# Performance work log

Hardware: AMD Instinct MI355X
Metric: run time of the kernel (lower is better)

The kernel has to match this reference:

```python
import jax, jax.numpy as jnp
import numpy as np

K_MASK = jnp.finfo(jnp.bfloat16).min
ROPE_THETA = 1000000.0


def _rope_sincos(position_ids, head_dim, theta):
    # position_ids: [b, t] int -> sin, cos: [b, t, head_dim//2]
    frac = jnp.arange(0, head_dim, 2, dtype=jnp.float32) / head_dim
    timescale = theta ** frac
    ang = position_ids[..., None].astype(jnp.float32) / timescale
    return jnp.sin(ang), jnp.cos(ang)


def _apply_rope(x, sin, cos):
    # x: [b, t, n, h]; sin/cos: [b, t, h//2]
    h = x.shape[-1]
    x1, x2 = x[..., : h // 2], x[..., h // 2 :]
    s = sin[:, :, None, :]
    c = cos[:, :, None, :]
    return jnp.concatenate([x1 * c - x2 * s, x2 * c + x1 * s], axis=-1).astype(x.dtype)


def setup_inputs() -> dict:
    key = jax.random.key(0)
    ks = jax.random.split(key, 8)
    b, t, S = 8, 16, 8192
    D, N, K, H = 1536, 12, 2, 128
    std = 0.01  # nnx.initializers.normal() default stddev
    return {
        "x": jax.random.normal(ks[0], (b, t, D), jnp.float32),
        "k_cache": jax.random.normal(ks[1], (b, S, K, H), jnp.float32),
        "v_cache": jax.random.normal(ks[2], (b, S, K, H), jnp.float32),
        "wq": jax.random.normal(ks[3], (D, N, H), jnp.float32) * std,
        "bq": jnp.zeros((N, H), jnp.float32),
        "wk": jax.random.normal(ks[4], (D, K, H), jnp.float32) * std,
        "bk": jnp.zeros((K, H), jnp.float32),
        "wv": jax.random.normal(ks[5], (D, K, H), jnp.float32) * std,
        "bv": jnp.zeros((K, H), jnp.float32),
        "wo": jax.random.normal(ks[6], (N, H, D), jnp.float32) * std,
        "segment_ids": jnp.ones((b, t), jnp.int32),
        "start_ind": jnp.zeros((8,), jnp.int32),
        "cur_ind": 4096,
    }


def reference(x, k_cache, v_cache, wq, bq, wk, bk, wv, bv, wo,
              segment_ids, start_ind, cur_ind):
    b, t, D = x.shape
    S = k_cache.shape[1]
    N, H = wq.shape[1], wq.shape[2]
    K = wk.shape[1]
    G = N // K  # n_rep
    scale = H ** -0.5

    # projections with bias
    q = jnp.einsum("btd,dnh->btnh", x, wq) + bq
    kp = jnp.einsum("btd,dkh->btkh", x, wk) + bk
    v = jnp.einsum("btd,dkh->btkh", x, wv) + bv

    # left-pad bookkeeping (count_left_pads) and start index resolution
    nonpad = segment_ids != 0  # [b, t]
    left_pads = jnp.argmax(nonpad, axis=-1).astype(jnp.int32)
    start = jnp.where(start_ind < 0, left_pads, start_ind)  # [b]

    # positions from segment ids, offset by current cache index
    positions = jnp.maximum(jnp.cumsum(nonpad.astype(jnp.int32), axis=-1) - 1, 0) + cur_ind
    sin, cos = _rope_sincos(positions, H, ROPE_THETA)
    q = _apply_rope(q, sin, cos)
    kp = _apply_rope(kp, sin, cos)

    # cache update
    k_cache = jax.lax.dynamic_update_slice(k_cache, kp.astype(k_cache.dtype), (0, cur_ind, 0, 0))
    v_cache = jax.lax.dynamic_update_slice(v_cache, v.astype(v_cache.dtype), (0, cur_ind, 0, 0))

    # GQA attention over full cache
    qg = q.reshape(b, t, K, G, H)
    logits = jnp.einsum("btkgh,bskh->btskg", qg, k_cache) * scale  # [b,t,S,K,G]

    q_pos = cur_ind + jnp.arange(t, dtype=jnp.int32)[None, :] - start[:, None]  # [b,t]
    ts = jnp.arange(S, dtype=jnp.int32)
    kv_seg = (ts[None, :] >= start[:, None]) & (ts[None, :] < cur_ind + t)  # [b,S]
    k_pos = ts[None, :] - start[:, None]
    causal = k_pos[:, None, :] <= q_pos[:, :, None]  # [b,t,S]
    seg = kv_seg[:, None, :].astype(segment_ids.dtype) == segment_ids[:, :, None]  # [b,t,S]
    mask = (causal & seg)[:, :, :, None, None]

    logits = jnp.where(mask, logits, K_MASK)
    w = jax.nn.softmax(logits.astype(jnp.float32), axis=2).astype(logits.dtype)
    qkv = jnp.einsum("btskg,bskh->btkgh", w, v_cache).reshape(b, t, N, H)
    return jnp.einsum("btnh,nhd->btd", qkv, wo)
```

## Files before the change

kernel.cpp:

```cpp
#include <hip/hip_runtime.h>
#include <hip/hip_bf16.h>

#define B_ 8
#define T_ 16
#define D_ 1536
#define N_ 12
#define KH_ 2
#define G_ 6
#define H_ 128
#define S_ 8192
#define NCHUNK 24
#define SPLITS 8
#define SKV 4160

typedef __attribute__((ext_vector_type(8))) short bf16x8;
typedef __attribute__((ext_vector_type(4))) float f32x4;
typedef __attribute__((ext_vector_type(4))) unsigned short u16x4;

__device__ __forceinline__ unsigned short f2bf(float x) {
    unsigned u = __float_as_uint(x);
    u += 0x7fffu + ((u >> 16) & 1u);
    return (unsigned short)(u >> 16);
}
__device__ __forceinline__ float bf2f(unsigned short h) {
    return __uint_as_float(((unsigned)h) << 16);
}

__global__ __launch_bounds__(256, 4) void gemm_splitk(
    const float* __restrict__ A,
    const float* __restrict__ W0, int n0, int ldb0,
    const float* __restrict__ W1, int n1, int ldb1,
    const float* __restrict__ W2, int ldb2,
    float* __restrict__ part, int NTOT, int Kdim)
{
    __shared__ __align__(16) unsigned short Ah[64][40], Al[64][40];
    __shared__ __align__(16) unsigned short Bh[64][40], Bl[64][40];
    const int tid = threadIdx.x;
    const int wave = tid >> 6, lane = tid & 63;
    const int col = lane & 15, g = lane >> 4;
    const int row0 = blockIdx.y * 64;
    const int c0 = blockIdx.x * 64;
    const int ks = Kdim / gridDim.z;
    const int k0 = blockIdx.z * ks;

    const float* Bp; int ldb, bc0;
    if (c0 < n0)           { Bp = W0; ldb = ldb0; bc0 = c0; }
    else if (c0 < n0 + n1) { Bp = W1; ldb = ldb1; bc0 = c0 - n0; }
    else                   { Bp = W2; ldb = ldb2; bc0 = c0 - n0 - n1; }

    f32x4 acc[4];
#pragma unroll
    for (int nt = 0; nt < 4; ++nt) acc[nt] = (f32x4){0.f, 0.f, 0.f, 0.f};

    for (int kk = 0; kk < ks; kk += 32) {
        __syncthreads();
        if (tid < 128) {
#pragma unroll
            for (int c = tid; c < 512; c += 128) {
                int r = c >> 3, k4 = c & 7;
                float4 v = *(const float4*)&A[(size_t)(row0 + r) * Kdim + k0 + kk + k4 * 4];
                float f[4] = {v.x, v.y, v.z, v.w};
                u16x4 hv, lv;
#pragma unroll
                for (int i = 0; i < 4; ++i) {
                    unsigned short hh = f2bf(f[i]);
                    hv[i] = hh; lv[i] = f2bf(f[i] - bf2f(hh));
                }
                *(u16x4*)&Ah[r][k4 * 4] = hv;
                *(u16x4*)&Al[r][k4 * 4] = lv;
            }
        } else {
            int t2 = tid - 128;
            int kq = t2 >> 4, cq = t2 & 15;
            float a[4][4];
#pragma unroll
            for (int r = 0; r < 4; ++r) {
                float4 v = *(const float4*)&Bp[(size_t)(k0 + kk + kq * 4 + r) * ldb + bc0 + cq * 4];
                a[r][0] = v.x; a[r][1] = v.y; a[r][2] = v.z; a[r][3] = v.w;
            }
#pragma unroll
            for (int cc = 0; cc < 4; ++cc) {
                u16x4 hv, lv;
#pragma unroll
                for (int r = 0; r < 4; ++r) {
                    unsigned short hh = f2bf(a[r][cc]);
                    hv[r] = hh; lv[r] = f2bf(a[r][cc] - bf2f(hh));
                }
                *(u16x4*)&Bh[cq * 4 + cc][kq * 4] = hv;
                *(u16x4*)&Bl[cq * 4 + cc][kq * 4] = lv;
            }
        }
        __syncthreads();

        bf16x8 ah = *(const bf16x8*)&Ah[wave * 16 + col][g * 8];
        bf16x8 al = *(const bf16x8*)&Al[wave * 16 + col][g * 8];
#pragma unroll
        for (int nt = 0; nt < 4; ++nt) {
            bf16x8 bh = *(const bf16x8*)&Bh[nt * 16 + col][g * 8];
            bf16x8 bl = *(const bf16x8*)&Bl[nt * 16 + col][g * 8];
            acc[nt] = __builtin_amdgcn_mfma_f32_16x16x32_bf16(ah, bh, acc[nt], 0, 0, 0);
            acc[nt] = __builtin_amdgcn_mfma_f32_16x16x32_bf16(ah, bl, acc[nt], 0, 0, 0);
            acc[nt] = __builtin_amdgcn_mfma_f32_16x16x32_bf16(al, bh, acc[nt], 0, 0, 0);
        }
    }
#pragma unroll
    for (int nt = 0; nt < 4; ++nt)
#pragma unroll
        for (int j = 0; j < 4; ++j) {
            size_t prow = (size_t)blockIdx.z * 128 + row0 + wave * 16 + g * 4 + j;
            part[prow * NTOT + c0 + nt * 16 + col] = acc[nt][j];
        }
}

__global__ __launch_bounds__(256) void rope_reduce(
    const float* __restrict__ part,
    const float* __restrict__ bq, const float* __restrict__ bk,
    const float* __restrict__ bv,
    const int* __restrict__ seg, const int* __restrict__ curp,
    float* __restrict__ q_rope, float* __restrict__ k_new,
    float* __restrict__ v_new)
{
    const int row = blockIdx.x;
    const int b = row >> 4, t = row & 15;
    const int tid = threadIdx.x;
    __shared__ float S[2048];
    __shared__ float sc[64][2];

    const int CUR = curp[0];
    int c = 0;
    for (int tt = 0; tt <= t; ++tt) c += (seg[b * T_ + tt] != 0) ? 1 : 0;
    int pos = max(c - 1, 0) + CUR;

    if (tid < 64) {
        float frac = (2.0f * tid) / (float)H_;
        float ts = expf(frac * logf(1000000.0f));
        float ang = (float)pos / ts;
        sc[tid][0] = sinf(ang);
        sc[tid][1] = cosf(ang);
    }
    for (int e = tid; e < 2048; e += 256) {
        float s = 0.f;
#pragma unroll
        for (int sp = 0; sp < SPLITS; ++sp)
            s += part[((size_t)sp * 128 + row) * 2048 + e];
        S[e] = s;
    }
    __syncthreads();

    for (int e = tid; e < 768; e += 256) {
        int n = e >> 6, i = e & 63;
        float x1 = S[n * 128 + i] + bq[n * 128 + i];
        float x2 = S[n * 128 + i + 64] + bq[n * 128 + i + 64];
        float s = sc[i][0], co = sc[i][1];
        q_rope[(size_t)row * 1536 + n * 128 + i]      = x1 * co - x2 * s;
        q_rope[(size_t)row * 1536 + n * 128 + i + 64] = x2 * co + x1 * s;
    }
    if (tid < 128) {
        int n = tid >> 6, i = tid & 63;
        float x1 = S[1536 + n * 128 + i] + bk[n * 128 + i];
        float x2 = S[1536 + n * 128 + i + 64] + bk[n * 128 + i + 64];
        float s = sc[i][0], co = sc[i][1];
        k_new[(size_t)row * 256 + n * 128 + i]      = x1 * co - x2 * s;
        k_new[(size_t)row * 256 + n * 128 + i + 64] = x2 * co + x1 * s;
    }
    v_new[(size_t)row * 256 + tid] = S[1792 + tid] + bv[tid];
}

__global__ __launch_bounds__(256) void pack_kv(
    const float* __restrict__ k_cache, const float* __restrict__ v_cache,
    const float* __restrict__ k_new, const float* __restrict__ v_new,
    const int* __restrict__ curp,
    unsigned short* __restrict__ Kb, unsigned short* __restrict__ Vtb)
{
    const int tile = blockIdx.x, b = blockIdx.y, kh = blockIdx.z;
    const int tid = threadIdx.x;
    const int CUR = curp[0], SPAN = CUR + T_;
    __shared__ float Vs[32][132];
    const int s_base = tile * 32;
    const int rr = tid >> 5, d0 = (tid & 31) * 4;
    const size_t kout = ((size_t)(b * KH_ + kh) * SKV + s_base) * H_;

#pragma unroll
    for (int i = 0; i < 4; ++i) {
        int r = rr + 8 * i;
        int s = min(s_base + r, SPAN - 1);
        const float* kr = (s < CUR)
            ? &k_cache[(((size_t)b * S_ + s) * KH_ + kh) * H_]
            : &k_new[(((size_t)b * T_ + (s - CUR)) * KH_ + kh) * H_];
        const float* vr = (s < CUR)
            ? &v_cache[(((size_t)b * S_ + s) * KH_ + kh) * H_]
            : &v_new[(((size_t)b * T_ + (s - CUR)) * KH_ + kh) * H_];
        float4 kv = *(const float4*)(kr + d0);
        u16x4 hk;
        hk[0] = f2bf(kv.x); hk[1] = f2bf(kv.y); hk[2] = f2bf(kv.z); hk[3] = f2bf(kv.w);
        *(u16x4*)&Kb[kout + (size_t)r * H_ + d0] = hk;
        *(float4*)&Vs[r][d0] = *(const float4*)(vr + d0);
    }
    __syncthreads();

    const int d = tid >> 1, kq = (tid & 1) * 16;
    unsigned short o[16];
#pragma unroll
    for (int i = 0; i < 16; ++i) o[i] = f2bf(Vs[kq + i][d]);
    unsigned short* vp = &Vtb[((size_t)(b * KH_ + kh) * H_ + d) * SKV + s_base + kq];
#pragma unroll
    for (int i = 0; i < 4; ++i)
        *(u16x4*)(vp + i * 4) = *(u16x4*)&o[i * 4];
}

__global__ __launch_bounds__(256, 3) void attn_mfma(
    const float* __restrict__ q_rope,
    const unsigned short* __restrict__ Kb,
    const unsigned short* __restrict__ Vtb,
    const int* __restrict__ seg, const int* __restrict__ start_ind,
    const int* __restrict__ curp,
    float* __restrict__ part)
{
    const int chunk = blockIdx.x, b = blockIdx.y;
    const int kh = blockIdx.z >> 1, half = blockIdx.z & 1;
    const int tid = threadIdx.x;
    const int wave = tid >> 6, lane = tid & 63;
    const int col = lane & 15, g = lane >> 4;
    const float scale = 0.088388347648318447f;
    const float NEG_INF = -__builtin_inff();

    const int CUR = curp[0];
    const int SPAN = CUR + T_;
    const int CH = (SPAN + NCHUNK - 1) / NCHUNK;
    const int s0 = chunk * CH;
    const int s1 = min(s0 + CH, SPAN);

    int st = start_ind[b];
    if (st < 0) {
        st = 0;
        for (int tt = 0; tt < T_; ++tt)
            if (seg[b * T_ + tt] != 0) { st = tt; break; }
    }

    __shared__ __align__(16) unsigned short Pl[4][16][40];

    const int qbase = half * 64 + wave * 16;
    const int qi_a = min(qbase + col, 95);
    const int t_a = (qi_a * 171) >> 10;
    const int gh_a = qi_a - t_a * G_;
    const float* qp = &q_rope[(((size_t)b * T_ + t_a) * N_ + kh * G_ + gh_a) * H_];
    bf16x8 qf[4];
#pragma unroll
    for (int ks = 0; ks < 4; ++ks) {
        float4 va = *(const float4*)&qp[ks * 32 + g * 8];
        float4 vb = *(const float4*)&qp[ks * 32 + g * 8 + 4];
        float f[8] = {va.x, va.y, va.z, va.w, vb.x, vb.y, vb.z, vb.w};
        union { bf16x8 v; __hip_bfloat162 h2[4]; } W;
#pragma unroll
        for (int i = 0; i < 4; ++i)
            W.h2[i] = __float22bfloat162_rn(make_float2(f[2 * i] * scale, f[2 * i + 1] * scale));
        qf[ks] = W.v;
    }

    int qpos_r[4], segid_r[4];
    bool wrow[4];
#pragma unroll
    for (int j = 0; j < 4; ++j) {
        int qi_raw = qbase + g * 4 + j;
        wrow[j] = (qi_raw < 96);
        int qi_c = min(qi_raw, 95);
        int t_c = (qi_c * 171) >> 10;
        segid_r[j] = seg[b * T_ + t_c];
        qpos_r[j] = CUR + t_c - st;
    }

    float m[4], lsum[4];
#pragma unroll
    for (int j = 0; j < 4; ++j) { m[j] = NEG_INF; lsum[j] = 0.f; }
    f32x4 oacc[8];
#pragma unroll
    for (int nt = 0; nt < 8; ++nt) oacc[nt] = (f32x4){0.f, 0.f, 0.f, 0.f};

    const unsigned short* Kbase = Kb + (size_t)(b * KH_ + kh) * SKV * H_;
    const unsigned short* Vbase = Vtb + (size_t)(b * KH_ + kh) * H_ * SKV;

    auto loadK = [&](bf16x8* kf, int stile) {
#pragma unroll
        for (int kt = 0; kt < 2; ++kt)
#pragma unroll
            for (int ks = 0; ks < 4; ++ks)
                kf[kt * 4 + ks] = *(const bf16x8*)
                    &Kbase[(size_t)(stile + kt * 16 + col) * H_ + ks * 32 + g * 8];
    };

    auto computeTile = [&](const bf16x8* kf, int stile) {
        f32x4 sacc0 = {0.f, 0.f, 0.f, 0.f}, sacc1 = {0.f, 0.f, 0.f, 0.f};
#pragma unroll
        for (int ks = 0; ks < 4; ++ks) {
            sacc0 = __builtin_amdgcn_mfma_f32_16x16x32_bf16(qf[ks], kf[ks], sacc0, 0, 0, 0);
            sacc1 = __builtin_amdgcn_mfma_f32_16x16x32_bf16(qf[ks], kf[4 + ks], sacc1, 0, 0, 0);
        }

        float rj[4];
        const int skey0 = stile + col, skey1 = stile + 16 + col;
#pragma unroll
        for (int j = 0; j < 4; ++j) {
            bool v0 = (skey0 < s1) && (skey0 - st <= qpos_r[j]) &&
                      (((skey0 >= st) ? 1 : 0) == segid_r[j]);
            bool v1 = (skey1 < s1) && (skey1 - st <= qpos_r[j]) &&
                      (((skey1 >= st) ? 1 : 0) == segid_r[j]);
            float lg0 = v0 ? sacc0[j] : NEG_INF;
            float lg1 = v1 ? sacc1[j] : NEG_INF;
            float tm = fmaxf(lg0, lg1);
            tm = fmaxf(tm, __shfl_xor(tm, 1));
            tm = fmaxf(tm, __shfl_xor(tm, 2));
            tm = fmaxf(tm, __shfl_xor(tm, 4));
            tm = fmaxf(tm, __shfl_xor(tm, 8));
            float mn = fmaxf(m[j], tm);
            float r, p0, p1;
            if (mn == NEG_INF) { r = 1.f; p0 = 0.f; p1 = 0.f; }
            else {
                r  = __expf(m[j] - mn);
                p0 = __expf(lg0 - mn);
                p1 = __expf(lg1 - mn);
            }
            float ps = p0 + p1;
            ps += __shfl_xor(ps, 1);
            ps += __shfl_xor(ps, 2);
            ps += __shfl_xor(ps, 4);
            ps += __shfl_xor(ps, 8);
            lsum[j] = lsum[j] * r + ps;
            m[j] = mn;
            rj[j] = r;
            int row = g * 4 + j;
            Pl[wave][row][col]      = f2bf(p0);
            Pl[wave][row][16 + col] = f2bf(p1);
        }

#pragma unroll
        for (int nt = 0; nt < 8; ++nt) {
#pragma unroll
            for (int j = 0; j < 4; ++j) oacc[nt][j] *= rj[j];
        }

        bf16x8 pa = *(const bf16x8*)&Pl[wave][col][g * 8];
#pragma unroll
        for (int nt = 0; nt < 8; ++nt) {
            bf16x8 vb = *(const bf16x8*)
                &Vbase[(size_t)(nt * 16 + col) * SKV + stile + g * 8];
            oacc[nt] = __builtin_amdgcn_mfma_f32_16x16x32_bf16(pa, vb, oacc[nt], 0, 0, 0);
        }
    };

    const int ntiles = (s1 - s0 + 31) >> 5;
    bf16x8 kfA[8], kfB[8];
    loadK(kfA, s0);
    for (int ti = 0; ti < ntiles; ti += 2) {
        if (ti + 1 < ntiles) loadK(kfB, s0 + (ti + 1) * 32);
        computeTile(kfA, s0 + ti * 32);
        if (ti + 1 < ntiles) {
            if (ti + 2 < ntiles) loadK(kfA, s0 + (ti + 2) * 32);
            computeTile(kfB, s0 + (ti + 1) * 32);
        }
    }

    const size_t base_q = (((size_t)chunk * B_ + b) * KH_ + kh) * 96;
#pragma unroll
    for (int j = 0; j < 4; ++j) {
        if (!wrow[j]) continue;
        int qi = qbase + g * 4 + j;
        size_t pb = (base_q + qi) * 132;
        if (col == 0) { part[pb] = m[j]; part[pb + 1] = lsum[j]; }
#pragma unroll
        for (int nt = 0; nt < 8; ++nt)
            part[pb + 2 + nt * 16 + col] = oacc[nt][j];
    }
}

__global__ __launch_bounds__(128) void combine_kernel(
    const float* __restrict__ part, float* __restrict__ qkv)
{
    const int qi = blockIdx.x, b = blockIdx.y, kh = blockIdx.z;
    const int h = threadIdx.x;
    const size_t cstride = (size_t)B_ * KH_ * 96 * 132;
    const size_t base0 = (((size_t)b * KH_ + kh) * 96 + qi) * 132;

    __shared__ float sm[NCHUNK], sl[NCHUNK];
    if (h < NCHUNK) {
        sm[h] = part[base0 + (size_t)h * cstride];
        sl[h] = part[base0 + (size_t)h * cstride + 1];
    }
    __syncthreads();

    float M = -__builtin_inff();
#pragma unroll
    for (int c = 0; c < NCHUNK; ++c) M = fmaxf(M, sm[c]);

    float den = 0.f, num = 0.f;
#pragma unroll
    for (int c = 0; c < NCHUNK; ++c) {
        float mc = sm[c];
        float e = (M == -__builtin_inff() || mc == -__builtin_inff())
                      ? 0.f : __expf(mc - M);
        den += e * sl[c];
        num += e * part[base0 + (size_t)c * cstride + 2 + h];
    }

    const int t = (qi * 171) >> 10;
    const int g = qi - t * G_;
    const int n = kh * G_ + g;
    qkv[(((size_t)b * T_ + t) * N_ + n) * H_ + h] = (den > 0.f) ? num / den : 0.f;
}

__global__ __launch_bounds__(256) void sum_reduce(
    const float* __restrict__ part, float* __restrict__ out, int n)
{
    int i = blockIdx.x * 256 + threadIdx.x;
    if (i < n) {
        float s = 0.f;
#pragma unroll
        for (int sp = 0; sp < SPLITS; ++sp) s += part[(size_t)sp * n + i];
        out[i] = s;
    }
}

extern "C" void kernel_launch(void* const* d_in, const int* in_sizes, int n_in,
                              void* d_out, int out_size, void* d_ws, size_t ws_size,
                              hipStream_t stream)
{
    (void)in_sizes; (void)n_in; (void)out_size; (void)ws_size;
    const float* x       = (const float*)d_in[0];
    const float* k_cache = (const float*)d_in[1];
    const float* v_cache = (const float*)d_in[2];
    const float* wq      = (const float*)d_in[3];
    const float* bq      = (const float*)d_in[4];
    const float* wk      = (const float*)d_in[5];
    const float* bk      = (const float*)d_in[6];
    const float* wv      = (const float*)d_in[7];
    const float* bv      = (const float*)d_in[8];
    const float* wo      = (const float*)d_in[9];
    const int*   seg     = (const int*)d_in[10];
    const int*   start_i = (const int*)d_in[11];
    const int*   curp    = (const int*)d_in[12];
    float* out = (float*)d_out;
    float* ws  = (float*)d_ws;

    const size_t PSZ  = (size_t)NCHUNK * B_ * KH_ * 96 * 132;
    const size_t QSZ  = (size_t)B_ * T_ * N_ * H_;
    const size_t KSZ  = (size_t)B_ * T_ * KH_ * H_;
    float* partP  = ws;
    float* partA  = ws;
    float* q_rope = ws + PSZ;
    float* k_new  = q_rope + QSZ;
    float* v_new  = k_new + KSZ;
    float* qkv    = v_new + KSZ;
    unsigned short* kvb = (unsigned short*)(qkv + QSZ);
    unsigned short* Kb  = kvb;
    unsigned short* Vtb = kvb + (size_t)B_ * KH_ * SKV * H_;

    gemm_splitk<<<dim3(32, 2, SPLITS), 256, 0, stream>>>(
        x, wq, 1536, 1536, wk, 256, 256, wv, 256, partP, 2048, D_);

    rope_reduce<<<B_ * T_, 256, 0, stream>>>(partP, bq, bk, bv, seg, curp,
                                             q_rope, k_new, v_new);

    pack_kv<<<dim3(SKV / 32, B_, KH_), 256, 0, stream>>>(
        k_cache, v_cache, k_new, v_new, curp, Kb, Vtb);

    attn_mfma<<<dim3(NCHUNK, B_, KH_ * 2), 256, 0, stream>>>(
        q_rope, Kb, Vtb, seg, start_i, curp, partA);

    combine_kernel<<<dim3(96, B_, KH_), 128, 0, stream>>>(partA, qkv);

    gemm_splitk<<<dim3(24, 2, SPLITS), 256, 0, stream>>>(
        qkv, wo, 1536, 1536, wo, 0, 1536, wo, 1536, partP, 1536, N_ * H_);

    sum_reduce<<<(B_ * T_ * D_ + 255) / 256, 256, 0, stream>>>(
        partP, out, B_ * T_ * D_);
}
```

Baseline: 112.3 us.

## Pack K/V into MFMA fragment-ordered tiles for coalesced attention loads

The pack kernel now writes K and V as per-32-key tiles laid out in the exact MFMA fragment order. Each lane of the attention kernel then reads contiguous 16-byte chunks from a single 16KB tile instead of strided rows from separate K and transposed V buffers. Chunk boundaries are rounded up to multiples of 32 so they align with tiles. V fragments are now loaded up front per tile, which raises register pressure, and the pack kernel uses more shared memory.

New measurement: 99.86 us. 11.0% less time.

```diff
diff --git a/kernel.cpp b/kernel.cpp
--- a/kernel.cpp
+++ b/kernel.cpp
@@ -12,6 +12,8 @@
 #define NCHUNK 24
 #define SPLITS 8
 #define SKV 4160
+#define NTILE (SKV / 32)
+#define TILE_USH 8192
 
 typedef __attribute__((ext_vector_type(8))) short bf16x8;
 typedef __attribute__((ext_vector_type(4))) float f32x4;
@@ -170,15 +172,14 @@
     const float* __restrict__ k_cache, const float* __restrict__ v_cache,
     const float* __restrict__ k_new, const float* __restrict__ v_new,
     const int* __restrict__ curp,
-    unsigned short* __restrict__ Kb, unsigned short* __restrict__ Vtb)
+    unsigned short* __restrict__ KVf)
 {
     const int tile = blockIdx.x, b = blockIdx.y, kh = blockIdx.z;
     const int tid = threadIdx.x;
     const int CUR = curp[0], SPAN = CUR + T_;
-    __shared__ float Vs[32][132];
+    __shared__ float Ks[32][133], Vsh[32][133];
     const int s_base = tile * 32;
     const int rr = tid >> 5, d0 = (tid & 31) * 4;
-    const size_t kout = ((size_t)(b * KH_ + kh) * SKV + s_base) * H_;
 
 #pragma unroll
     for (int i = 0; i < 4; ++i) {
@@ -190,28 +191,48 @@
         const float* vr = (s < CUR)
             ? &v_cache[(((size_t)b * S_ + s) * KH_ + kh) * H_]
             : &v_new[(((size_t)b * T_ + (s - CUR)) * KH_ + kh) * H_];
-        float4 kv = *(const float4*)(kr + d0);
-        u16x4 hk;
-        hk[0] = f2bf(kv.x); hk[1] = f2bf(kv.y); hk[2] = f2bf(kv.z); hk[3] = f2bf(kv.w);
-        *(u16x4*)&Kb[kout + (size_t)r * H_ + d0] = hk;
-        *(float4*)&Vs[r][d0] = *(const float4*)(vr + d0);
+        *(float4*)&Ks[r][d0]  = *(const float4*)(kr + d0);
+        *(float4*)&Vsh[r][d0] = *(const float4*)(vr + d0);
     }
     __syncthreads();
 
-    const int d = tid >> 1, kq = (tid & 1) * 16;
-    unsigned short o[16];
-#pragma unroll
-    for (int i = 0; i < 16; ++i) o[i] = f2bf(Vs[kq + i][d]);
-    unsigned short* vp = &Vtb[((size_t)(b * KH_ + kh) * H_ + d) * SKV + s_base + kq];
-#pragma unroll
-    for (int i = 0; i < 4; ++i)
-        *(u16x4*)(vp + i * 4) = *(u16x4*)&o[i * 4];
+    unsigned short* KT = KVf + ((size_t)(b * KH_ + kh) * NTILE + tile) * TILE_USH;
+    unsigned short* VT = KT + 4096;
+
+#pragma unroll
+    for (int hw = 0; hw < 2; ++hw) {
+        const int w = tid + hw * 256;
+        const int f = w >> 6, l = w & 63;
+        const int col = l & 15, g = l >> 4;
+        {
+            const int key = (f >> 2) * 16 + col;
+            const int dim = (f & 3) * 32 + g * 8;
+            u16x4 o0, o1;
+#pragma unroll
+            for (int e = 0; e < 4; ++e) {
+                o0[e] = f2bf(Ks[key][dim + e]);
+                o1[e] = f2bf(Ks[key][dim + 4 + e]);
+            }
+            *(u16x4*)&KT[(size_t)w * 8]     = o0;
+            *(u16x4*)&KT[(size_t)w * 8 + 4] = o1;
+        }
+        {
+            const int dim = f * 16 + col;
+            u16x4 o0, o1;
+#pragma unroll
+            for (int e = 0; e < 4; ++e) {
+                o0[e] = f2bf(Vsh[g * 8 + e][dim]);
+                o1[e] = f2bf(Vsh[g * 8 + 4 + e][dim]);
+            }
+            *(u16x4*)&VT[(size_t)w * 8]     = o0;
+            *(u16x4*)&VT[(size_t)w * 8 + 4] = o1;
+        }
+    }
 }
 
 __global__ __launch_bounds__(256, 3) void attn_mfma(
     const float* __restrict__ q_rope,
-    const unsigned short* __restrict__ Kb,
-    const unsigned short* __restrict__ Vtb,
+    const unsigned short* __restrict__ KVf,
     const int* __restrict__ seg, const int* __restrict__ start_ind,
     const int* __restrict__ curp,
     float* __restrict__ part)
@@ -226,7 +247,7 @@
 
     const int CUR = curp[0];
     const int SPAN = CUR + T_;
-    const int CH = (SPAN + NCHUNK - 1) / NCHUNK;
+    const int CH = (((SPAN + NCHUNK - 1) / NCHUNK) + 31) & ~31;
     const int s0 = chunk * CH;
     const int s1 = min(s0 + CH, SPAN);
 
@@ -276,19 +297,22 @@
 #pragma unroll
     for (int nt = 0; nt < 8; ++nt) oacc[nt] = (f32x4){0.f, 0.f, 0.f, 0.f};
 
-    const unsigned short* Kbase = Kb + (size_t)(b * KH_ + kh) * SKV * H_;
-    const unsigned short* Vbase = Vtb + (size_t)(b * KH_ + kh) * H_ * SKV;
-
-    auto loadK = [&](bf16x8* kf, int stile) {
-#pragma unroll
-        for (int kt = 0; kt < 2; ++kt)
-#pragma unroll
-            for (int ks = 0; ks < 4; ++ks)
-                kf[kt * 4 + ks] = *(const bf16x8*)
-                    &Kbase[(size_t)(stile + kt * 16 + col) * H_ + ks * 32 + g * 8];
+    const unsigned short* KVbase = KVf + (size_t)(b * KH_ + kh) * NTILE * TILE_USH;
+
+    auto loadK = [&](bf16x8* kf, int tileIdx) {
+        const unsigned short* KT = KVbase + (size_t)tileIdx * TILE_USH;
+#pragma unroll
+        for (int f = 0; f < 8; ++f)
+            kf[f] = *(const bf16x8*)&KT[(f * 64 + lane) * 8];
     };
 
-    auto computeTile = [&](const bf16x8* kf, int stile) {
+    auto computeTile = [&](const bf16x8* kf, int tileIdx, int stile) {
+        const unsigned short* VT = KVbase + (size_t)tileIdx * TILE_USH + 4096;
+        bf16x8 vfr[8];
+#pragma unroll
+        for (int f = 0; f < 8; ++f)
+            vfr[f] = *(const bf16x8*)&VT[(f * 64 + lane) * 8];
+
         f32x4 sacc0 = {0.f, 0.f, 0.f, 0.f}, sacc1 = {0.f, 0.f, 0.f, 0.f};
 #pragma unroll
         for (int ks = 0; ks < 4; ++ks) {
@@ -340,22 +364,21 @@
 
         bf16x8 pa = *(const bf16x8*)&Pl[wave][col][g * 8];
 #pragma unroll
-        for (int nt = 0; nt < 8; ++nt) {
-            bf16x8 vb = *(const bf16x8*)
-                &Vbase[(size_t)(nt * 16 + col) * SKV + stile + g * 8];
-            oacc[nt] = __builtin_amdgcn_mfma_f32_16x16x32_bf16(pa, vb, oacc[nt], 0, 0, 0);
-        }
+        for (int nt = 0; nt < 8; ++nt)
+            oacc[nt] = __builtin_amdgcn_mfma_f32_16x16x32_bf16(pa, vfr[nt], oacc[nt], 0, 0, 0);
     };
 
-    const int ntiles = (s1 - s0 + 31) >> 5;
+    const int nt_raw = (s1 - s0 + 31) >> 5;
+    const int ntiles = (s1 > s0) ? nt_raw : 0;
+    const int tile0 = s0 >> 5;
     bf16x8 kfA[8], kfB[8];
-    loadK(kfA, s0);
+    if (ntiles > 0) loadK(kfA, tile0);
     for (int ti = 0; ti < ntiles; ti += 2) {
-        if (ti + 1 < ntiles) loadK(kfB, s0 + (ti + 1) * 32);
-        computeTile(kfA, s0 + ti * 32);
+        if (ti + 1 < ntiles) loadK(kfB, tile0 + ti + 1);
+        computeTile(kfA, tile0 + ti, s0 + ti * 32);
         if (ti + 1 < ntiles) {
-            if (ti + 2 < ntiles) loadK(kfA, s0 + (ti + 2) * 32);
-            computeTile(kfB, s0 + (ti + 1) * 32);
+            if (ti + 2 < ntiles) loadK(kfA, tile0 + ti + 2);
+            computeTile(kfB, tile0 + ti + 1, s0 + (ti + 1) * 32);
         }
     }
 
@@ -449,9 +472,7 @@
     float* k_new  = q_rope + QSZ;
     float* v_new  = k_new + KSZ;
     float* qkv    = v_new + KSZ;
-    unsigned short* kvb = (unsigned short*)(qkv + QSZ);
-    unsigned short* Kb  = kvb;
-    unsigned short* Vtb = kvb + (size_t)B_ * KH_ * SKV * H_;
+    unsigned short* KVf = (unsigned short*)(qkv + QSZ);
 
     gemm_splitk<<<dim3(32, 2, SPLITS), 256, 0, stream>>>(
         x, wq, 1536, 1536, wk, 256, 256, wv, 256, partP, 2048, D_);
@@ -459,11 +480,11 @@
     rope_reduce<<<B_ * T_, 256, 0, stream>>>(partP, bq, bk, bv, seg, curp,
                                              q_rope, k_new, v_new);
 
-    pack_kv<<<dim3(SKV / 32, B_, KH_), 256, 0, stream>>>(
-        k_cache, v_cache, k_new, v_new, curp, Kb, Vtb);
+    pack_kv<<<dim3(NTILE, B_, KH_), 256, 0, stream>>>(
+        k_cache, v_cache, k_new, v_new, curp, KVf);
 
     attn_mfma<<<dim3(NCHUNK, B_, KH_ * 2), 256, 0, stream>>>(
-        q_rope, Kb, Vtb, seg, start_i, curp, partA);
+        q_rope, KVf, seg, start_i, curp, partA);
 
     combine_kernel<<<dim3(96, B_, KH_), 128, 0, stream>>>(partA, qkv);
 
```
